# Optimization experiments

Measured on AMD Instinct MI355X. Metric: run time of the kernel, lower is better.

The kernel has to match this reference:

```python
import jax, jax.numpy as jnp
import numpy as np

IN_CAPS, IN_DIMS = 32, 288
OUT_CAPS, OUT_DIMS = 10, 16
N_ITERS = 3


def setup_inputs() -> dict:
    key = jax.random.key(0)
    k1, k2 = jax.random.split(key)
    B = 8192
    data = jax.random.normal(k1, (B, IN_CAPS, IN_DIMS), dtype=jnp.float32)
    stdv = 1.0 / 32.0
    W = jax.random.uniform(k2, (IN_CAPS, IN_DIMS, OUT_CAPS * OUT_DIMS),
                           dtype=jnp.float32, minval=-stdv, maxval=stdv)
    return {"data": data, "W": W}


def reference(data, W):
    B = data.shape[0]
    # u_hat[b,i,o,d]: per-input-capsule predictions for each output capsule
    u_hat = jnp.einsum('bci,cio->bco', data, W).reshape(B, IN_CAPS, OUT_CAPS, OUT_DIMS)
    b = jnp.zeros((IN_CAPS, OUT_CAPS), dtype=u_hat.dtype)
    v = None
    for _ in range(N_ITERS):  # fixed small iteration count
        c = jax.nn.softmax(b, axis=0)                      # (IN_CAPS, OUT_CAPS), softmax over input capsules
        v = jnp.einsum('io,biod->bod', c, u_hat)           # (B, OUT_CAPS, OUT_DIMS)
        # agreement: sqrt of sum of squared elementwise products, averaged over batch
        a = jnp.sqrt(jnp.sum((u_hat * v[:, None, :, :]) ** 2, axis=-1)).mean(axis=0)
        b = b + a
    return v
```

## Files before the change

### kernel.cpp

```cpp
#include <hip/hip_runtime.h>
#include <hip/hip_bf16.h>

#define NB 8192
#define IC 32
#define ID 288
#define OD16 160

typedef __attribute__((ext_vector_type(8))) short bf16x8;
typedef __attribute__((ext_vector_type(4))) float f32x4;

__device__ __forceinline__ unsigned short f2bf(float f) {
    unsigned int u = __builtin_bit_cast(unsigned int, f);
    u = u + 0x7fffu + ((u >> 16) & 1u);
    return (unsigned short)(u >> 16);
}
__device__ __forceinline__ float bf2f(unsigned short h) {
    return __builtin_bit_cast(float, ((unsigned int)h) << 16);
}
__device__ __forceinline__ bf16x8 cvt_bf8(const f32x4& a, const f32x4& b) {
    union { __hip_bfloat162 h[4]; bf16x8 v; } u;
    u.h[0] = __float22bfloat162_rn(make_float2(a[0], a[1]));
    u.h[1] = __float22bfloat162_rn(make_float2(a[2], a[3]));
    u.h[2] = __float22bfloat162_rn(make_float2(b[0], b[1]));
    u.h[3] = __float22bfloat162_rn(make_float2(b[2], b[3]));
    return u.v;
}

__device__ __forceinline__ void gld_lds16(const void* g, void* l) {
    __builtin_amdgcn_global_load_lds((const __attribute__((address_space(1))) unsigned int*)g,
                                     (__attribute__((address_space(3))) unsigned int*)l, 16, 0, 0);
}

__global__ __launch_bounds__(256) void prep_kernel(const float* __restrict__ W,
                                                   unsigned short* __restrict__ WtImg,
                                                   float* __restrict__ a_arr) {
    __shared__ short tile[160 * 72];
    const int bx = blockIdx.x;
    const int c = bx / 5;
    const int s = bx - c * 5;
    const int t = threadIdx.x;
    if (bx == 0) {
        for (int i = t; i < 3 * 8 * 320; i += 256) a_arr[i] = 0.f;
    }
    const int kw = (s == 4) ? 32 : 64;
    const int nel = kw * 160;
    for (int idx = t; idx < nel; idx += 256) {
        int k = idx / 160;
        int n = idx - k * 160;
        tile[n * 72 + k] = (short)f2bf(W[((long)c * ID + s * 64 + k) * OD16 + n]);
    }
    __syncthreads();
    unsigned short* dst = WtImg + ((long)c * 5 + s) * 10240;
    for (int p = t; p < 1280; p += 256) {
        int n = p >> 3;
        int g = (p & 7) ^ (n & 7);
        uint4 val = make_uint4(0u, 0u, 0u, 0u);
        if (g * 8 < kw) val = *(const uint4*)&tile[n * 72 + g * 8];
        *(uint4*)(dst + p * 8) = val;
    }
}

__global__ __launch_bounds__(256) void gemm_kernel(const float* __restrict__ data,
                                                   const unsigned short* __restrict__ WtImg,
                                                   unsigned short* __restrict__ uhat) {
    __shared__ alignas(16) char lds[73728];
    char* const Alds = lds;
    char* const Blds = lds + 32768;
    const int tid = threadIdx.x;
    const int lane = tid & 63;
    const int w = tid >> 6;
    const int q = lane >> 4;
    const int r = lane & 15;
    const int b0 = blockIdx.x * 128;
    const int cc = blockIdx.y;

    const float* Ag = data + (long)(b0 + w * 32 + (lane >> 3)) * (IC * ID) + cc * ID
                      + ((lane & 7) ^ ((lane >> 3) & 7)) * 4;
    const unsigned short* Wc = WtImg + (long)cc * 51200;

    f32x4 acc[2][10];
    #pragma unroll
    for (int i = 0; i < 2; ++i)
        #pragma unroll
        for (int j = 0; j < 10; ++j)
            acc[i][j] = (f32x4){0.f, 0.f, 0.f, 0.f};

    auto issueA = [&](int buf, int kc) {
        char* dst = Alds + w * 8192 + buf * 4096;
        const float* src = Ag + kc * 32;
        #pragma unroll
        for (int j = 0; j < 4; ++j)
            gld_lds16(src + (long)j * 8 * (IC * ID), dst + j * 1024);
    };
    auto issueB = [&](int buf, int s) {
        const unsigned short* src = Wc + s * 10240 + (w * 5) * 512 + lane * 8;
        char* dst = Blds + buf * 20480 + (w * 5) * 1024;
        #pragma unroll
        for (int j = 0; j < 5; ++j)
            gld_lds16(src + j * 512, dst + j * 1024);
    };

#define COMPUTE(KC)                                                            \
    {                                                                          \
        const char* Ab = Alds + w * 8192 + ((KC) & 1) * 4096;                  \
        const char* Bb = Blds + (((KC) >> 1) & 1) * 20480;                     \
        const int kb = ((KC) & 1) * 64 + q * 16;                               \
        bf16x8 bfr[10];                                                        \
        _Pragma("unroll")                                                      \
        for (int nf = 0; nf < 10; ++nf) {                                      \
            const int n = nf * 16 + r;                                         \
            bfr[nf] = *(const bf16x8*)(Bb + ((n * 128 + kb) ^ ((n & 7) << 4)));\
        }                                                                      \
        bf16x8 af[2];                                                          \
        _Pragma("unroll")                                                      \
        for (int mf = 0; mf < 2; ++mf) {                                       \
            const int row = mf * 16 + r;                                       \
            const int c0 = (q * 2) ^ (r & 7);                                  \
            const int c1 = (q * 2 + 1) ^ (r & 7);                              \
            f32x4 alo = *(const f32x4*)(Ab + row * 128 + c0 * 16);             \
            f32x4 ahi = *(const f32x4*)(Ab + row * 128 + c1 * 16);             \
            af[mf] = cvt_bf8(alo, ahi);                                        \
        }                                                                      \
        _Pragma("unroll")                                                      \
        for (int nf = 0; nf < 10; ++nf) {                                      \
            acc[0][nf] = __builtin_amdgcn_mfma_f32_16x16x32_bf16(af[0], bfr[nf], acc[0][nf], 0, 0, 0); \
            acc[1][nf] = __builtin_amdgcn_mfma_f32_16x16x32_bf16(af[1], bfr[nf], acc[1][nf], 0, 0, 0); \
        }                                                                      \
    }

#define WAITV(N)  { asm volatile("s_waitcnt vmcnt(" N ")" ::: "memory");       \
                    __builtin_amdgcn_sched_barrier(0); }
#define BAR()     { __builtin_amdgcn_s_barrier(); }

    issueA(0, 0); issueB(0, 0); issueA(1, 1); issueB(1, 1);
    WAITV("9") BAR() COMPUTE(0)
    issueA(0, 2); WAITV("9") COMPUTE(1) BAR()
    issueA(1, 3); issueB(0, 2); WAITV("9") BAR() COMPUTE(2)
    issueA(0, 4); WAITV("9") COMPUTE(3) BAR()
    issueA(1, 5); issueB(1, 3); WAITV("9") BAR() COMPUTE(4)
    issueA(0, 6); WAITV("9") COMPUTE(5) BAR()
    issueA(1, 7); issueB(0, 4); WAITV("9") BAR() COMPUTE(6)
    issueA(0, 8); WAITV("9") COMPUTE(7) BAR()
    WAITV("0") BAR() COMPUTE(8)

#undef COMPUTE
#undef WAITV
#undef BAR

    __syncthreads();
    short* eb = (short*)Blds;
    #pragma unroll
    for (int mf = 0; mf < 2; ++mf)
        #pragma unroll
        for (int rr = 0; rr < 4; ++rr) {
            const int m = w * 32 + mf * 16 + (q << 2) + rr;
            #pragma unroll
            for (int nf = 0; nf < 10; ++nf)
                eb[m * 160 + nf * 16 + r] = (short)f2bf(acc[mf][nf][rr]);
        }
    __syncthreads();
    unsigned short* dstc = uhat + ((long)cc * NB + b0) * 160;
    #pragma unroll
    for (int j = 0; j < 10; ++j) {
        const int chunk = j * 256 + tid;
        *(uint4*)(dstc + chunk * 8) = *(const uint4*)(eb + chunk * 8);
    }
}

template <int COMPUTE_A, int WRITE_V>
__global__ __launch_bounds__(256) void route_kernel(const unsigned short* __restrict__ uhat,
                                                    const float* __restrict__ a_all,
                                                    int n_prev,
                                                    float* __restrict__ a_out,
                                                    float* __restrict__ v_out) {
    constexpr long PL = (long)NB * 160;
    __shared__ float c_sh[320];
    __shared__ float v_lds[4][160];
    __shared__ float a_sh[4][320];
    const int tid = threadIdx.x;
    for (int base = 0; base < 320; base += 256) {
        int t = base + tid;
        if (t < 320) {
            float bv = 0.f;
            for (int j = 0; j < n_prev * 8; ++j) bv += a_all[j * 320 + t];
            bv *= (1.0f / 8192.0f);
            float m = bv;
            #pragma unroll
            for (int off = 1; off < 32; off <<= 1) m = fmaxf(m, __shfl_xor(m, off));
            float e = __expf(bv - m);
            float ssum = e;
            #pragma unroll
            for (int off = 1; off < 32; off <<= 1) ssum += __shfl_xor(ssum, off);
            c_sh[t] = e / ssum;
        }
    }
    __syncthreads();

    const int w = tid >> 6;
    const int lane = tid & 63;
    const long row = (long)blockIdx.x * 4 + w;
    const unsigned short* __restrict__ u = uhat + row * 160;

    ushort4 ua[5][4];
    if (COMPUTE_A) {
        #pragma unroll
        for (int s5 = 0; s5 < 5; ++s5) {
            const int i = lane & 31;
            const int oo = (lane >> 5) + 2 * s5;
            #pragma unroll
            for (int d4 = 0; d4 < 4; ++d4)
                ua[s5][d4] = *(const ushort4*)(u + (long)i * PL + oo * 16 + d4 * 4);
        }
    }

    if (lane < 40) {
        const int q = lane;
        const int o = q >> 2;
        float4 sv = {0.f, 0.f, 0.f, 0.f};
        #pragma unroll 8
        for (int i = 0; i < 32; ++i) {
            ushort4 uu = *(const ushort4*)(u + (long)i * PL + q * 4);
            float ci = c_sh[o * 32 + i];
            sv.x += ci * bf2f(uu.x);
            sv.y += ci * bf2f(uu.y);
            sv.z += ci * bf2f(uu.z);
            sv.w += ci * bf2f(uu.w);
        }
        if (WRITE_V) *(float4*)(v_out + row * 160 + q * 4) = sv;
        if (COMPUTE_A) *(float4*)(&v_lds[w][q * 4]) = sv;
    }

    if (COMPUTE_A) {
        asm volatile("s_waitcnt lgkmcnt(0)" ::: "memory");
        #pragma unroll
        for (int s5 = 0; s5 < 5; ++s5) {
            const int i = lane & 31;
            const int oo = (lane >> 5) + 2 * s5;
            const float* vp = &v_lds[w][oo * 16];
            float accv = 0.f;
            #pragma unroll
            for (int d4 = 0; d4 < 4; ++d4) {
                ushort4 uu = ua[s5][d4];
                float4 vv = *(const float4*)(vp + d4 * 4);
                float p0 = bf2f(uu.x) * vv.x;
                float p1 = bf2f(uu.y) * vv.y;
                float p2 = bf2f(uu.z) * vv.z;
                float p3 = bf2f(uu.w) * vv.w;
                accv += p0 * p0 + p1 * p1 + p2 * p2 + p3 * p3;
            }
            a_sh[w][oo * 32 + i] = sqrtf(accv);
        }
        __syncthreads();
        for (int t = tid; t < 320; t += 256) {
            float s4 = a_sh[0][t] + a_sh[1][t] + a_sh[2][t] + a_sh[3][t];
            atomicAdd(a_out + (blockIdx.x & 7) * 320 + t, s4);
        }
    }
}

extern "C" void kernel_launch(void* const* d_in, const int* in_sizes, int n_in,
                              void* d_out, int out_size, void* d_ws, size_t ws_size,
                              hipStream_t stream) {
    const float* data = (const float*)d_in[0];
    const float* W = (const float*)d_in[1];
    float* out = (float*)d_out;
    char* ws = (char*)d_ws;

    unsigned short* uhat = (unsigned short*)ws;
    size_t off = (size_t)NB * IC * OD16 * 2;
    unsigned short* WtImg = (unsigned short*)(ws + off);
    off += 32L * 5 * 10240 * 2;
    float* a_arr = (float*)(ws + off); off += 3 * 8 * 320 * 4;

    hipLaunchKernelGGL(prep_kernel, dim3(160), dim3(256), 0, stream, W, WtImg, a_arr);
    hipLaunchKernelGGL(gemm_kernel, dim3(64, 32), dim3(256), 0, stream, data, WtImg, uhat);
    hipLaunchKernelGGL((route_kernel<1, 0>), dim3(2048), dim3(256), 0, stream,
                       uhat, a_arr, 0, a_arr + 0 * 2560, out);
    hipLaunchKernelGGL((route_kernel<1, 0>), dim3(2048), dim3(256), 0, stream,
                       uhat, a_arr, 1, a_arr + 1 * 2560, out);
    hipLaunchKernelGGL((route_kernel<0, 1>), dim3(2048), dim3(256), 0, stream,
                       uhat, a_arr, 2, a_arr + 2 * 2560, out);
}
```

Baseline: 165.5 us.

## Stage W per 32-wide k-chunk with smaller LDS buffers and padded epilogue

The pre-transposed bf16 W image is re-laid out in 32-wide k chunks (9 per input capsule) with a new XOR swizzle. The GEMM now double-buffers B per k-chunk alongside A instead of per 64-wide slab. This cuts LDS use from 72 KB to 52 KB, which may let more blocks fit per CU, at the cost of an extra barrier per step. The epilogue staging buffer gets a padded row stride of 168 to reduce LDS bank conflicts.

```diff
diff --git a/kernel.cpp b/kernel.cpp
--- a/kernel.cpp
+++ b/kernel.cpp
@@ -32,7 +32,7 @@
 }
 
 __global__ __launch_bounds__(256) void prep_kernel(const float* __restrict__ W,
-                                                   unsigned short* __restrict__ WtImg,
+                                                   unsigned short* __restrict__ Bimg,
                                                    float* __restrict__ a_arr) {
     __shared__ short tile[160 * 72];
     const int bx = blockIdx.x;
@@ -50,20 +50,23 @@
         tile[n * 72 + k] = (short)f2bf(W[((long)c * ID + s * 64 + k) * OD16 + n]);
     }
     __syncthreads();
-    unsigned short* dst = WtImg + ((long)c * 5 + s) * 10240;
-    for (int p = t; p < 1280; p += 256) {
-        int n = p >> 3;
-        int g = (p & 7) ^ (n & 7);
-        uint4 val = make_uint4(0u, 0u, 0u, 0u);
-        if (g * 8 < kw) val = *(const uint4*)&tile[n * 72 + g * 8];
-        *(uint4*)(dst + p * 8) = val;
+    unsigned short* dst0 = Bimg + ((long)c * 9 + s * 2) * (160 * 32);
+    const int nkc = (s == 4) ? 1 : 2;
+    for (int kcl = 0; kcl < nkc; ++kcl) {
+        unsigned short* dst = dst0 + kcl * (160 * 32);
+        for (int p = t; p < 640; p += 256) {
+            int n = p >> 2;
+            int sl = p & 3;
+            int g = sl ^ ((n >> 1) & 3);
+            *(uint4*)(dst + p * 8) = *(const uint4*)&tile[n * 72 + kcl * 32 + g * 8];
+        }
     }
 }
 
 __global__ __launch_bounds__(256) void gemm_kernel(const float* __restrict__ data,
-                                                   const unsigned short* __restrict__ WtImg,
+                                                   const unsigned short* __restrict__ Bimg,
                                                    unsigned short* __restrict__ uhat) {
-    __shared__ alignas(16) char lds[73728];
+    __shared__ alignas(16) char lds[53248];
     char* const Alds = lds;
     char* const Blds = lds + 32768;
     const int tid = threadIdx.x;
@@ -76,7 +79,7 @@
 
     const float* Ag = data + (long)(b0 + w * 32 + (lane >> 3)) * (IC * ID) + cc * ID
                       + ((lane & 7) ^ ((lane >> 3) & 7)) * 4;
-    const unsigned short* Wc = WtImg + (long)cc * 51200;
+    const unsigned short* Bc = Bimg + (long)cc * (9 * 160 * 32);
 
     f32x4 acc[2][10];
     #pragma unroll
@@ -92,25 +95,23 @@
         for (int j = 0; j < 4; ++j)
             gld_lds16(src + (long)j * 8 * (IC * ID), dst + j * 1024);
     };
-    auto issueB = [&](int buf, int s) {
-        const unsigned short* src = Wc + s * 10240 + (w * 5) * 512 + lane * 8;
-        char* dst = Blds + buf * 20480 + (w * 5) * 1024;
-        #pragma unroll
-        for (int j = 0; j < 5; ++j)
-            gld_lds16(src + j * 512, dst + j * 1024);
+    auto issueB = [&](int buf, int kc) {
+        const unsigned short* src = Bc + kc * (160 * 32) + (w * 160 + lane) * 8;
+        char* dst = Blds + buf * 10240 + w * 2560;
+        gld_lds16(src, dst);
+        gld_lds16(src + 64 * 8, dst + 1024);
+        if (lane < 32) gld_lds16(src + 128 * 8, dst + 2048);
     };
 
 #define COMPUTE(KC)                                                            \
     {                                                                          \
         const char* Ab = Alds + w * 8192 + ((KC) & 1) * 4096;                  \
-        const char* Bb = Blds + (((KC) >> 1) & 1) * 20480;                     \
-        const int kb = ((KC) & 1) * 64 + q * 16;                               \
+        const char* Bb = Blds + ((KC) & 1) * 10240;                            \
+        const int slot = q ^ ((r >> 1) & 3);                                   \
         bf16x8 bfr[10];                                                        \
         _Pragma("unroll")                                                      \
-        for (int nf = 0; nf < 10; ++nf) {                                      \
-            const int n = nf * 16 + r;                                         \
-            bfr[nf] = *(const bf16x8*)(Bb + ((n * 128 + kb) ^ ((n & 7) << 4)));\
-        }                                                                      \
+        for (int nf = 0; nf < 10; ++nf)                                        \
+            bfr[nf] = *(const bf16x8*)(Bb + (nf * 16 + r) * 64 + slot * 16);   \
         bf16x8 af[2];                                                          \
         _Pragma("unroll")                                                      \
         for (int mf = 0; mf < 2; ++mf) {                                       \
@@ -133,14 +134,14 @@
 #define BAR()     { __builtin_amdgcn_s_barrier(); }
 
     issueA(0, 0); issueB(0, 0); issueA(1, 1); issueB(1, 1);
-    WAITV("9") BAR() COMPUTE(0)
-    issueA(0, 2); WAITV("9") COMPUTE(1) BAR()
-    issueA(1, 3); issueB(0, 2); WAITV("9") BAR() COMPUTE(2)
-    issueA(0, 4); WAITV("9") COMPUTE(3) BAR()
-    issueA(1, 5); issueB(1, 3); WAITV("9") BAR() COMPUTE(4)
-    issueA(0, 6); WAITV("9") COMPUTE(5) BAR()
-    issueA(1, 7); issueB(0, 4); WAITV("9") BAR() COMPUTE(6)
-    issueA(0, 8); WAITV("9") COMPUTE(7) BAR()
+    WAITV("7") BAR() COMPUTE(0) BAR()
+    issueA(0, 2); issueB(0, 2); WAITV("7") BAR() COMPUTE(1) BAR()
+    issueA(1, 3); issueB(1, 3); WAITV("7") BAR() COMPUTE(2) BAR()
+    issueA(0, 4); issueB(0, 4); WAITV("7") BAR() COMPUTE(3) BAR()
+    issueA(1, 5); issueB(1, 5); WAITV("7") BAR() COMPUTE(4) BAR()
+    issueA(0, 6); issueB(0, 6); WAITV("7") BAR() COMPUTE(5) BAR()
+    issueA(1, 7); issueB(1, 7); WAITV("7") BAR() COMPUTE(6) BAR()
+    issueA(0, 8); issueB(0, 8); WAITV("7") BAR() COMPUTE(7)
     WAITV("0") BAR() COMPUTE(8)
 
 #undef COMPUTE
@@ -148,7 +149,7 @@
 #undef BAR
 
     __syncthreads();
-    short* eb = (short*)Blds;
+    short* eb = (short*)lds;
     #pragma unroll
     for (int mf = 0; mf < 2; ++mf)
         #pragma unroll
@@ -156,14 +157,16 @@
             const int m = w * 32 + mf * 16 + (q << 2) + rr;
             #pragma unroll
             for (int nf = 0; nf < 10; ++nf)
-                eb[m * 160 + nf * 16 + r] = (short)f2bf(acc[mf][nf][rr]);
+                eb[m * 168 + nf * 16 + r] = (short)f2bf(acc[mf][nf][rr]);
         }
     __syncthreads();
     unsigned short* dstc = uhat + ((long)cc * NB + b0) * 160;
     #pragma unroll
     for (int j = 0; j < 10; ++j) {
         const int chunk = j * 256 + tid;
-        *(uint4*)(dstc + chunk * 8) = *(const uint4*)(eb + chunk * 8);
+        const int row = chunk / 20;
+        const int p = chunk - row * 20;
+        *(uint4*)(dstc + (long)row * 160 + p * 8) = *(const uint4*)(eb + row * 168 + p * 8);
     }
 }
 
@@ -268,12 +271,12 @@
 
     unsigned short* uhat = (unsigned short*)ws;
     size_t off = (size_t)NB * IC * OD16 * 2;
-    unsigned short* WtImg = (unsigned short*)(ws + off);
-    off += 32L * 5 * 10240 * 2;
+    unsigned short* Bimg = (unsigned short*)(ws + off);
+    off += 32L * 9 * 160 * 32 * 2;
     float* a_arr = (float*)(ws + off); off += 3 * 8 * 320 * 4;
 
-    hipLaunchKernelGGL(prep_kernel, dim3(160), dim3(256), 0, stream, W, WtImg, a_arr);
-    hipLaunchKernelGGL(gemm_kernel, dim3(64, 32), dim3(256), 0, stream, data, WtImg, uhat);
+    hipLaunchKernelGGL(prep_kernel, dim3(160), dim3(256), 0, stream, W, Bimg, a_arr);
+    hipLaunchKernelGGL(gemm_kernel, dim3(64, 32), dim3(256), 0, stream, data, Bimg, uhat);
     hipLaunchKernelGGL((route_kernel<1, 0>), dim3(2048), dim3(256), 0, stream,
                        uhat, a_arr, 0, a_arr + 0 * 2560, out);
     hipLaunchKernelGGL((route_kernel<1, 0>), dim3(2048), dim3(256), 0, stream,
```

Result: no change. 164.9 us (-0.4%).
